# Kernel tuning notes

Hardware: AMD Instinct MI355X
Metric: run time of the kernel (lower is better)

Reference implementation:

```python
import jax, jax.numpy as jnp
import numpy as np

D_MODEL = 1024
N_HEADS = 16
D_HEAD = D_MODEL // N_HEADS
B, T = 4, 2048


def setup_inputs() -> dict:
    key = jax.random.key(0)
    k1, k2, k3 = jax.random.split(key, 3)
    x = jax.random.normal(k1, (B, T, D_MODEL), dtype=jnp.float32)
    # causal mask, broadcastable [1,1,T,T]; 0 => masked
    mask = jnp.tril(jnp.ones((T, T), dtype=jnp.int32))[None, None, :, :]
    # torch Linear weight is [out,in]; store transposed for x @ W
    Wqkv = jax.random.normal(k2, (D_MODEL, 3 * D_MODEL), dtype=jnp.float32) * (D_MODEL ** -0.5)
    Wout = jax.random.normal(k3, (D_MODEL, D_MODEL), dtype=jnp.float32) * (D_MODEL ** -0.5)
    return {"x": x, "mask": mask, "Wqkv": Wqkv, "Wout": Wout}


def reference(x, mask, Wqkv, Wout):
    Bb, Tt, C = x.shape
    qkv = (x @ Wqkv).reshape(Bb, Tt, 3, N_HEADS, D_HEAD)
    qkv = jnp.transpose(qkv, (2, 0, 3, 1, 4))  # [3,B,H,T,Dh]
    q, k, v = qkv[0], qkv[1], qkv[2]
    scale = 1.0 / jnp.sqrt(jnp.asarray(D_HEAD, x.dtype))
    att = jnp.einsum("bhqd,bhkd->bhqk", q, k) * scale  # [B,H,T,T]
    att = jnp.where(mask[:, :, :Tt, :Tt] == 0, jnp.asarray(-jnp.inf, att.dtype), att)
    att = jax.nn.softmax(att, axis=-1)
    out = jnp.einsum("bhqk,bhkd->bhqd", att, v)  # [B,H,T,Dh]
    out = jnp.transpose(out, (0, 2, 1, 3)).reshape(Bb, Tt, C)
    return out @ Wout
```

## Files before the change

kernel.cpp:

```cpp
#include <hip/hip_runtime.h>
#include <hip/hip_bf16.h>

#define BATCH   4
#define SEQ     2048
#define DMODEL  1024
#define NHEADS  16
#define DHEAD   64
#define BT      (BATCH*SEQ)

typedef unsigned short u16;
typedef unsigned int u32;
typedef __bf16 bf16x8 __attribute__((ext_vector_type(8)));
typedef float  f32x4  __attribute__((ext_vector_type(4)));
typedef float  f32x16 __attribute__((ext_vector_type(16)));
typedef u16    u16x8  __attribute__((ext_vector_type(8)));
typedef u16    u16x4  __attribute__((ext_vector_type(4)));
typedef u32    u32x4  __attribute__((ext_vector_type(4)));

#define MFMA16(a,b,c) __builtin_amdgcn_mfma_f32_16x16x32_bf16((a),(b),(c),0,0,0)
#define MFMA32(a,b,c) __builtin_amdgcn_mfma_f32_32x32x16_bf16((a),(b),(c),0,0,0)

__device__ __forceinline__ u16 f2b(float f) {
  return __builtin_bit_cast(u16, (__bf16)f);
}
__device__ __forceinline__ u32 pack2(float lo, float hi) {
  return (u32)f2b(lo) | ((u32)f2b(hi) << 16);
}

__device__ __forceinline__ void gload_lds16(const u16* g, u16* l) {
  __builtin_amdgcn_global_load_lds(
      (const __attribute__((address_space(1))) void*)g,
      (__attribute__((address_space(3))) void*)l, 16, 0, 0);
}

__global__ __launch_bounds__(256) void cvt_bf16_kernel(
    const float* __restrict__ in, u16* __restrict__ out, int n8) {
  int i = blockIdx.x * 256 + threadIdx.x;
  if (i >= n8) return;
  const float4* p = (const float4*)(in + (long)i * 8);
  float4 a = p[0], b = p[1];
  u16x8 o;
  o[0]=f2b(a.x); o[1]=f2b(a.y); o[2]=f2b(a.z); o[3]=f2b(a.w);
  o[4]=f2b(b.x); o[5]=f2b(b.y); o[6]=f2b(b.z); o[7]=f2b(b.w);
  *(u16x8*)(out + (long)i * 8) = o;
}

__global__ __launch_bounds__(256) void transpose_cvt_kernel(
    const float* __restrict__ W, u16* __restrict__ Wt, int K, int N) {
  __shared__ float tile[32][33];
  int tx = threadIdx.x & 31, ty = threadIdx.x >> 5;
  int bx = blockIdx.x, by = blockIdx.y;
  #pragma unroll
  for (int r = 0; r < 32; r += 8)
    tile[ty + r][tx] = W[(long)(by * 32 + ty + r) * N + bx * 32 + tx];
  __syncthreads();
  #pragma unroll
  for (int r = 0; r < 32; r += 8)
    Wt[(long)(bx * 32 + ty + r) * K + by * 32 + tx] = f2b(tile[tx][ty + r]);
}

template<int MODE>
__global__ __launch_bounds__(256) void gemm_bt_kernel(
    const u16* __restrict__ A, const u16* __restrict__ Bt,
    float* __restrict__ C,
    u16* __restrict__ Qb, u16* __restrict__ Kb, u16* __restrict__ Vt,
    int M, int N, int K) {
  __shared__ u16 lA[128 * 32];
  __shared__ u16 lB[128 * 32];
  const int tid = threadIdx.x;
  const int l = tid & 63, w = tid >> 6;
  const int g = l >> 4, c16 = l & 15;
  const int bn = blockIdx.x, bm = blockIdx.y;
  const int wm = w >> 1, wn = w & 1;
  const int srow = tid >> 2;
  const int scol = (tid & 3) << 3;
  const u16* Ab0 = A  + (long)(bm * 128 + srow)      * K + scol;
  const u16* Ab1 = A  + (long)(bm * 128 + 64 + srow) * K + scol;
  const u16* Bb0 = Bt + (long)(bn * 128 + srow)      * K + scol;
  const u16* Bb1 = Bt + (long)(bn * 128 + 64 + srow) * K + scol;
  u16* lA0 = &lA[srow * 32 + scol];
  u16* lA1 = &lA[(64 + srow) * 32 + scol];
  u16* lB0 = &lB[srow * 32 + scol];
  u16* lB1 = &lB[(64 + srow) * 32 + scol];

  f32x4 acc[4][4];
  #pragma unroll
  for (int i = 0; i < 4; ++i)
    #pragma unroll
    for (int j = 0; j < 4; ++j)
      #pragma unroll
      for (int e = 0; e < 4; ++e) acc[i][j][e] = 0.f;

  for (int k0 = 0; k0 < K; k0 += 32) {
    gload_lds16(Ab0 + k0, lA0);
    gload_lds16(Ab1 + k0, lA1);
    gload_lds16(Bb0 + k0, lB0);
    gload_lds16(Bb1 + k0, lB1);
    __syncthreads();
    bf16x8 af[4];
    #pragma unroll
    for (int mf = 0; mf < 4; ++mf)
      af[mf] = *(const bf16x8*)&lA[(wm * 64 + mf * 16 + c16) * 32 + g * 8];
    #pragma unroll
    for (int nf = 0; nf < 4; ++nf) {
      bf16x8 bfr = *(const bf16x8*)&lB[(wn * 64 + nf * 16 + c16) * 32 + g * 8];
      #pragma unroll
      for (int mf = 0; mf < 4; ++mf)
        acc[mf][nf] = MFMA16(af[mf], bfr, acc[mf][nf]);
    }
    __syncthreads();
  }

  #pragma unroll
  for (int mf = 0; mf < 4; ++mf) {
    const int trow_base = bm * 128 + wm * 64 + mf * 16 + g * 4;
    #pragma unroll
    for (int nf = 0; nf < 4; ++nf) {
      const int col = bn * 128 + wn * 64 + nf * 16 + c16;
      #pragma unroll
      for (int r = 0; r < 4; ++r) {
        const float v = acc[mf][nf][r];
        const int trow = trow_base + r;
        if constexpr (MODE == 0) {
          C[(long)trow * N + col] = v;
        } else {
          const int s = col >> 10;
          const int rem = col & 1023;
          const int h = rem >> 6, d = rem & 63;
          const int b = trow >> 11, tt = trow & 2047;
          const int bh = b * NHEADS + h;
          if (s == 0)      Qb[((long)bh * SEQ + tt) * DHEAD + d] = f2b(v * 0.125f);
          else if (s == 1) Kb[((long)bh * SEQ + tt) * DHEAD + d] = f2b(v);
          else             Vt[((long)bh * DHEAD + d) * SEQ + tt] = f2b(v);
        }
      }
    }
  }
}

__global__ __launch_bounds__(512, 2) void attn_kernel(
    const u16* __restrict__ Qb, const u16* __restrict__ Kb,
    const u16* __restrict__ Vt, u16* __restrict__ Ob) {
  __shared__ u16 kbuf[2][64 * 64];
  __shared__ u16 vbuf[2][64 * 64];
  const int tid = threadIdx.x;
  const int lane = tid & 63, w = tid >> 6;
  const int c = lane & 31, g2 = lane >> 5;
  const int bh = blockIdx.x;
  const int b = bh >> 4, h = bh & 15;
  const u16* Kbh = Kb + (long)bh * SEQ * DHEAD;
  const u16* Vbh = Vt + (long)bh * DHEAD * SEQ;

  const int srow = lane >> 3;
  const int sswz = ((lane & 7) * 16) ^ (srow << 4);
  const int swz  = (c & 7) << 4;

  #pragma unroll 1
  for (int pass = 0; pass < 2; ++pass) {
    const int qblk = pass ? (7 - (int)blockIdx.y) : (int)blockIdx.y;
    const int qb0 = qblk * 256;
    const int qrow0 = qb0 + w * 32;
    const int nt = qb0 / 64 + 4;
    const int mytiles = (qrow0 + 31) / 64 + 1;

    bf16x8 qf[4];
    {
      const u16* Qrow = Qb + ((long)bh * SEQ + qrow0 + c) * DHEAD + g2 * 8;
      #pragma unroll
      for (int ds = 0; ds < 4; ++ds)
        qf[ds] = *(const bf16x8*)(Qrow + ds * 16);
    }

    f32x16 o0, o1;
    #pragma unroll
    for (int e = 0; e < 16; ++e) { o0[e] = 0.f; o1[e] = 0.f; }
    float m_run = -__builtin_inff(), l_run = 0.f;

    {
      const u16* gk = Kbh + (long)(w * 8 + srow) * DHEAD + (sswz >> 1);
      gload_lds16(gk, &kbuf[0][w * 512]);
      const u16* gv = Vbh + (long)(w * 8 + srow) * SEQ + (sswz >> 1);
      gload_lds16(gv, &vbuf[0][w * 512]);
    }
    asm volatile("s_waitcnt vmcnt(0)" ::: "memory");
    __builtin_amdgcn_s_barrier();

    #pragma unroll 1
    for (int t = 0; t < nt; ++t) {
      const int kv = t * 64;
      const int cur = t & 1;
      if (t + 1 < nt) {
        const int kv2 = kv + 64;
        const u16* gk = Kbh + (long)(kv2 + w * 8 + srow) * DHEAD + (sswz >> 1);
        gload_lds16(gk, &kbuf[cur ^ 1][w * 512]);
        const u16* gv = Vbh + (long)(w * 8 + srow) * SEQ + kv2 + (sswz >> 1);
        gload_lds16(gv, &vbuf[cur ^ 1][w * 512]);
        asm volatile("s_waitcnt vmcnt(2)" ::: "memory");
      } else {
        asm volatile("s_waitcnt vmcnt(0)" ::: "memory");
      }
      __builtin_amdgcn_s_barrier();

      if (t < mytiles) {
        f32x16 p0, p1;
        #pragma unroll
        for (int e = 0; e < 16; ++e) { p0[e] = 0.f; p1[e] = 0.f; }
        const char* kb = (const char*)&kbuf[cur][0];
        __builtin_amdgcn_s_setprio(1);
        #pragma unroll
        for (int ds = 0; ds < 4; ++ds) {
          bf16x8 aK0 = *(const bf16x8*)(kb + c * 128 + ((ds * 32 + g2 * 16) ^ swz));
          bf16x8 aK1 = *(const bf16x8*)(kb + (32 + c) * 128 + ((ds * 32 + g2 * 16) ^ swz));
          p0 = MFMA32(aK0, qf[ds], p0);
          p1 = MFMA32(aK1, qf[ds], p1);
        }
        __builtin_amdgcn_s_setprio(0);

        if (kv + 63 > qrow0) {
          const int q = qrow0 + c;
          #pragma unroll
          for (int r = 0; r < 16; ++r) {
            const int koff = (r & 3) + 8 * (r >> 2) + 4 * g2;
            if (kv + koff > q)      p0[r] = -__builtin_inff();
            if (kv + 32 + koff > q) p1[r] = -__builtin_inff();
          }
        }

        float vmax = p0[0];
        #pragma unroll
        for (int e = 1; e < 16; ++e) vmax = fmaxf(vmax, p0[e]);
        #pragma unroll
        for (int e = 0; e < 16; ++e) vmax = fmaxf(vmax, p1[e]);
        vmax = fmaxf(vmax, __shfl_xor(vmax, 32, 64));
        const float mnew = fmaxf(m_run, vmax);
        const float scale = __builtin_amdgcn_exp2f((m_run - mnew) * 1.44269504f);
        m_run = mnew;
        float ps = 0.f;
        #pragma unroll
        for (int e = 0; e < 16; ++e) {
          p0[e] = __builtin_amdgcn_exp2f((p0[e] - mnew) * 1.44269504f);
          p1[e] = __builtin_amdgcn_exp2f((p1[e] - mnew) * 1.44269504f);
          ps += p0[e] + p1[e];
        }
        ps += __shfl_xor(ps, 32, 64);
        l_run = l_run * scale + ps;
        #pragma unroll
        for (int e = 0; e < 16; ++e) { o0[e] *= scale; o1[e] *= scale; }

        u32x4 pbw[4];
        #pragma unroll
        for (int s = 0; s < 4; ++s) {
          const int base = 8 * (s & 1);
          float e0, e1, e2, e3, e4, e5, e6, e7;
          if (s < 2) {
            e0=p0[base+0]; e1=p0[base+1]; e2=p0[base+2]; e3=p0[base+3];
            e4=p0[base+4]; e5=p0[base+5]; e6=p0[base+6]; e7=p0[base+7];
          } else {
            e0=p1[base+0]; e1=p1[base+1]; e2=p1[base+2]; e3=p1[base+3];
            e4=p1[base+4]; e5=p1[base+5]; e6=p1[base+6]; e7=p1[base+7];
          }
          const u32 w01 = pack2(e0, e1), w23 = pack2(e2, e3);
          const u32 w45 = pack2(e4, e5), w67 = pack2(e6, e7);
          const u32 sendA = g2 ? w01 : w45;
          const u32 sendB = g2 ? w23 : w67;
          const u32 recvA = (u32)__shfl_xor((int)sendA, 32, 64);
          const u32 recvB = (u32)__shfl_xor((int)sendB, 32, 64);
          pbw[s][0] = g2 ? recvA : w01;
          pbw[s][1] = g2 ? recvB : w23;
          pbw[s][2] = g2 ? w45 : recvA;
          pbw[s][3] = g2 ? w67 : recvB;
        }

        const char* vb = (const char*)&vbuf[cur][0];
        __builtin_amdgcn_s_setprio(1);
        #pragma unroll
        for (int s = 0; s < 4; ++s) {
          const bf16x8 pv = __builtin_bit_cast(bf16x8, pbw[s]);
          bf16x8 aV0 = *(const bf16x8*)(vb + c * 128 + ((s * 32 + g2 * 16) ^ swz));
          bf16x8 aV1 = *(const bf16x8*)(vb + (32 + c) * 128 + ((s * 32 + g2 * 16) ^ swz));
          o0 = MFMA32(aV0, pv, o0);
          o1 = MFMA32(aV1, pv, o1);
        }
        __builtin_amdgcn_s_setprio(0);
      }
      asm volatile("" ::: "memory");
      __builtin_amdgcn_s_barrier();
    }

    const float rinv = 1.f / l_run;
    const int q = qrow0 + c;
    u16* orow = Ob + ((long)b * SEQ + q) * DMODEL + h * DHEAD;
    #pragma unroll
    for (int m = 0; m < 4; ++m) {
      u16x4 v0, v1;
      #pragma unroll
      for (int e = 0; e < 4; ++e) {
        v0[e] = f2b(o0[4 * m + e] * rinv);
        v1[e] = f2b(o1[4 * m + e] * rinv);
      }
      const int d0 = 8 * m + 4 * g2;
      *(u16x4*)(orow + d0) = v0;
      *(u16x4*)(orow + 32 + d0) = v1;
    }
  }
}

extern "C" void kernel_launch(void* const* d_in, const int* in_sizes, int n_in,
                              void* d_out, int out_size, void* d_ws, size_t ws_size,
                              hipStream_t stream) {
  const float* x    = (const float*)d_in[0];
  const float* Wqkv = (const float*)d_in[2];
  const float* Wout = (const float*)d_in[3];
  float* out = (float*)d_out;
  char* ws = (char*)d_ws;
  u16* Xb  = (u16*)(ws + 0);
  u16* Wt1 = (u16*)(ws + 16777216);
  u16* Wt2 = (u16*)(ws + 23068672);
  u16* Qb  = (u16*)(ws + 25165824);
  u16* Kb  = (u16*)(ws + 41943040);
  u16* Vt  = (u16*)(ws + 58720256);
  u16* Ob  = (u16*)(ws + 75497472);

  cvt_bf16_kernel<<<4096, 256, 0, stream>>>(x, Xb, BT * DMODEL / 8);
  transpose_cvt_kernel<<<dim3(96, 32), 256, 0, stream>>>(Wqkv, Wt1, DMODEL, 3 * DMODEL);
  transpose_cvt_kernel<<<dim3(32, 32), 256, 0, stream>>>(Wout, Wt2, DMODEL, DMODEL);
  gemm_bt_kernel<1><<<dim3(24, 64), 256, 0, stream>>>(
      Xb, Wt1, nullptr, Qb, Kb, Vt, BT, 3 * DMODEL, DMODEL);
  attn_kernel<<<dim3(64, 4), 512, 0, stream>>>(Qb, Kb, Vt, Ob);
  gemm_bt_kernel<0><<<dim3(8, 64), 256, 0, stream>>>(
      Ob, Wt2, out, nullptr, nullptr, nullptr, BT, DMODEL, DMODEL);
}
```

Before: 304.6 us.

## Double-buffer GEMM LDS tiles with K=64 steps and XOR-swizzled layout

Rewrites the GEMM main loop to use two LDS buffers, each holding a 128x64 K-slice, and prefetches the next slice while computing on the current one, with explicit vmcnt waits. The LDS layout is XOR-swizzled to avoid bank conflicts on the fragment reads, and setprio raises wave priority around the MFMA block. The intent is to hide global-load latency and halve the number of barriers per K, at the cost of four times the LDS per block, which may lower occupancy.

```diff
diff --git a/kernel.cpp b/kernel.cpp
--- a/kernel.cpp
+++ b/kernel.cpp
@@ -65,23 +65,19 @@
     float* __restrict__ C,
     u16* __restrict__ Qb, u16* __restrict__ Kb, u16* __restrict__ Vt,
     int M, int N, int K) {
-  __shared__ u16 lA[128 * 32];
-  __shared__ u16 lB[128 * 32];
+  __shared__ u16 lA[2][128 * 64];
+  __shared__ u16 lB[2][128 * 64];
   const int tid = threadIdx.x;
   const int l = tid & 63, w = tid >> 6;
   const int g = l >> 4, c16 = l & 15;
   const int bn = blockIdx.x, bm = blockIdx.y;
   const int wm = w >> 1, wn = w & 1;
-  const int srow = tid >> 2;
-  const int scol = (tid & 3) << 3;
-  const u16* Ab0 = A  + (long)(bm * 128 + srow)      * K + scol;
-  const u16* Ab1 = A  + (long)(bm * 128 + 64 + srow) * K + scol;
-  const u16* Bb0 = Bt + (long)(bn * 128 + srow)      * K + scol;
-  const u16* Bb1 = Bt + (long)(bn * 128 + 64 + srow) * K + scol;
-  u16* lA0 = &lA[srow * 32 + scol];
-  u16* lA1 = &lA[(64 + srow) * 32 + scol];
-  u16* lB0 = &lB[srow * 32 + scol];
-  u16* lB1 = &lB[(64 + srow) * 32 + scol];
+  const int srow = tid >> 3;
+  const int sslot = tid & 7;
+  const int scol = ((sslot ^ (srow & 7)) << 3);
+  const u16* Ab = A  + (long)(bm * 128 + srow) * K + scol;
+  const u16* Bb = Bt + (long)(bn * 128 + srow) * K + scol;
+  const int ldst = srow * 64 + sslot * 8;
 
   f32x4 acc[4][4];
   #pragma unroll
@@ -91,24 +87,56 @@
       #pragma unroll
       for (int e = 0; e < 4; ++e) acc[i][j][e] = 0.f;
 
-  for (int k0 = 0; k0 < K; k0 += 32) {
-    gload_lds16(Ab0 + k0, lA0);
-    gload_lds16(Ab1 + k0, lA1);
-    gload_lds16(Bb0 + k0, lB0);
-    gload_lds16(Bb1 + k0, lB1);
-    __syncthreads();
-    bf16x8 af[4];
-    #pragma unroll
-    for (int mf = 0; mf < 4; ++mf)
-      af[mf] = *(const bf16x8*)&lA[(wm * 64 + mf * 16 + c16) * 32 + g * 8];
-    #pragma unroll
-    for (int nf = 0; nf < 4; ++nf) {
-      bf16x8 bfr = *(const bf16x8*)&lB[(wn * 64 + nf * 16 + c16) * 32 + g * 8];
+  const int nt = K >> 6;
+  #pragma unroll
+  for (int h = 0; h < 4; ++h) {
+    gload_lds16(Ab + (long)h * 32 * K, &lA[0][h * 32 * 64 + ldst]);
+    gload_lds16(Bb + (long)h * 32 * K, &lB[0][h * 32 * 64 + ldst]);
+  }
+  asm volatile("s_waitcnt vmcnt(0)" ::: "memory");
+  __builtin_amdgcn_s_barrier();
+
+  #pragma unroll 1
+  for (int t = 0; t < nt; ++t) {
+    const int cur = t & 1;
+    if (t + 1 < nt) {
+      const long koff = (long)(t + 1) * 64;
+      #pragma unroll
+      for (int h = 0; h < 4; ++h) {
+        gload_lds16(Ab + (long)h * 32 * K + koff, &lA[cur ^ 1][h * 32 * 64 + ldst]);
+        gload_lds16(Bb + (long)h * 32 * K + koff, &lB[cur ^ 1][h * 32 * 64 + ldst]);
+      }
+      asm volatile("s_waitcnt vmcnt(8)" ::: "memory");
+    } else {
+      asm volatile("s_waitcnt vmcnt(0)" ::: "memory");
+    }
+    __builtin_amdgcn_s_barrier();
+    asm volatile("" ::: "memory");
+
+    const char* a0 = (const char*)&lA[cur][0];
+    const char* b0 = (const char*)&lB[cur][0];
+    const int swz = (c16 & 7) << 4;
+    __builtin_amdgcn_s_setprio(1);
+    #pragma unroll
+    for (int ks = 0; ks < 2; ++ks) {
+      bf16x8 af[4], bfr[4];
       #pragma unroll
       for (int mf = 0; mf < 4; ++mf)
-        acc[mf][nf] = MFMA16(af[mf], bfr, acc[mf][nf]);
-    }
-    __syncthreads();
+        af[mf] = *(const bf16x8*)(a0 + (wm * 64 + mf * 16 + c16) * 128 +
+                                  (((ks * 4 + g) * 16) ^ swz));
+      #pragma unroll
+      for (int nf = 0; nf < 4; ++nf)
+        bfr[nf] = *(const bf16x8*)(b0 + (wn * 64 + nf * 16 + c16) * 128 +
+                                   (((ks * 4 + g) * 16) ^ swz));
+      #pragma unroll
+      for (int nf = 0; nf < 4; ++nf)
+        #pragma unroll
+        for (int mf = 0; mf < 4; ++mf)
+          acc[mf][nf] = MFMA16(af[mf], bfr[nf], acc[mf][nf]);
+    }
+    __builtin_amdgcn_s_setprio(0);
+    asm volatile("" ::: "memory");
+    __builtin_amdgcn_s_barrier();
   }
 
   #pragma unroll
```

Result: faster. 296.8 us (-2.5%).
